# Kernel optimization log

Measured on AMD Instinct MI355X. Metric: run time of the kernel, lower is better.

## Reference

```python
import jax, jax.numpy as jnp
import numpy as np

B, L, D_IN, H = 16, 2048, 1024, 512  # bidirectional: out_size = 2*H = D_IN (k=3 SRU layout)


def setup_inputs() -> dict:
    key = jax.random.key(0)
    k1, k2, k3, k4 = jax.random.split(key, 4)
    x = jax.random.normal(k1, (B, L, D_IN), dtype=jnp.float32)
    W = jax.random.normal(k2, (D_IN, 2, H, 3), dtype=jnp.float32) * 0.02
    bf = jax.random.normal(k3, (2, H), dtype=jnp.float32) * 0.02
    br = jax.random.normal(k4, (2, H), dtype=jnp.float32) * 0.02
    return {"x": x, "W": W, "bf": bf, "br": br}


def _sru_scan(xtil, f, r, xres, reverse):
    # xtil/f/r/xres: (L, B, H). Diagonal linear recurrence:
    #   c_t = f_t * c_{t-1} + (1 - f_t) * xtil_t
    #   h_t = r_t * tanh(c_t) + (1 - r_t) * xres_t
    def step(c, inp):
        xt_, f_, r_, xr_ = inp
        c = f_ * c + (1.0 - f_) * xt_
        h = r_ * jnp.tanh(c) + (1.0 - r_) * xr_
        return c, h
    c0 = jnp.zeros(xtil.shape[1:], dtype=xtil.dtype)
    c_last, h = jax.lax.scan(step, c0, (xtil, f, r, xres), reverse=reverse)
    return h, c_last


def reference(x, W, bf, br):
    xt = jnp.transpose(x, (1, 0, 2))  # (L, B, D_IN), as the wrapper does x.transpose(0,1)
    # U: (L, B, 2 dirs, H, 3 = [x_tilde, f_pre, r_pre])
    U = jnp.einsum("lbi,idhk->lbdhk", xt, W)
    f = jax.nn.sigmoid(U[..., 1] + bf[None, None, :, :])  # (L,B,2,H)
    r = jax.nn.sigmoid(U[..., 2] + br[None, None, :, :])
    xtil = U[..., 0]
    # highway/residual: raw input split per direction since n_in == 2*H (k=3)
    xres = xt.reshape(L, B, 2, H)

    h_f, c_f = _sru_scan(xtil[:, :, 0], f[:, :, 0], r[:, :, 0], xres[:, :, 0], reverse=False)
    h_b, c_b = _sru_scan(xtil[:, :, 1], f[:, :, 1], r[:, :, 1], xres[:, :, 1], reverse=True)

    h = jnp.concatenate([h_f, h_b], axis=-1)          # (L, B, 2H)
    c = jnp.concatenate([c_f, c_b], axis=-1)          # (B, 2H) final cell states
    # wrapper returns (out.transpose(0,1), c.transpose(0,1))
    return jnp.transpose(h, (1, 0, 2)), c.T
```

## Files before the change

### kernel.cpp

```cpp
#include <hip/hip_runtime.h>
#include <stdint.h>

#define B_    16
#define L_    2048
#define DIN_  1024
#define H_    512
#define NCOL_ 3072
#define M_    (B_ * L_)
#define K_    DIN_
#define NCHUNK 16
#define CHUNK  128

typedef unsigned short u16;
typedef __bf16 bf16_t;
typedef bf16_t bf16x8 __attribute__((ext_vector_type(8)));
typedef float  f32x4  __attribute__((ext_vector_type(4)));

__device__ __forceinline__ u16 f2bf(float f) {
  union { float f; uint32_t u; } v; v.f = f;
  return (u16)((v.u + 0x7fffu + ((v.u >> 16) & 1u)) >> 16);
}
__device__ __forceinline__ float bf2f(u16 b) {
  union { uint32_t u; float f; } v; v.u = ((uint32_t)b) << 16; return v.f;
}
__device__ __forceinline__ u16 f2h(float f) {
  _Float16 h = (_Float16)f; return *(u16*)&h;
}
__device__ __forceinline__ float h2f(u16 b) {
  _Float16 h = *(_Float16*)&b; return (float)h;
}

__global__ void cvt_x_kernel(const float4* __restrict__ x, ushort4* __restrict__ xb) {
  int i = blockIdx.x * blockDim.x + threadIdx.x;
  float4 v = x[i];
  ushort4 o;
  o.x = f2bf(v.x); o.y = f2bf(v.y); o.z = f2bf(v.z); o.w = f2bf(v.w);
  xb[i] = o;
}

__global__ void transpose_w_kernel(const float* __restrict__ W, u16* __restrict__ Wt) {
  __shared__ float s[32][33];
  int n0 = blockIdx.x * 32;
  int i0 = blockIdx.y * 32;
  int tx = threadIdx.x, ty = threadIdx.y;
  #pragma unroll
  for (int y = 0; y < 32; y += 8)
    s[ty + y][tx] = W[(uint64_t)(i0 + ty + y) * NCOL_ + n0 + tx];
  __syncthreads();
  #pragma unroll
  for (int y = 0; y < 32; y += 8) {
    int n = n0 + ty + y;
    int kk = n % 3, d = n / 1536, h = (n % 1536) / 3;
    int np = kk * 1024 + d * 512 + h;
    Wt[(uint64_t)np * K_ + i0 + tx] = f2bf(s[tx][ty + y]);
  }
}

__device__ __forceinline__ void gload_lds16(const void* g, void* lds) {
  __builtin_amdgcn_global_load_lds(
      (const __attribute__((address_space(1))) uint32_t*)g,
      (__attribute__((address_space(3))) uint32_t*)lds, 16, 0, 0);
}

__device__ __forceinline__ bf16x8 lds_rd(const u16* lds, int byteOff) {
  return __builtin_bit_cast(bf16x8, *(const f32x4*)((const char*)lds + byteOff));
}

__global__ __launch_bounds__(256, 2) void gemm_u_kernel(const u16* __restrict__ A,
                                                        const u16* __restrict__ Bt,
                                                        const float* __restrict__ bfp,
                                                        const float* __restrict__ brp,
                                                        u16* __restrict__ xtilP,
                                                        u16* __restrict__ fP,
                                                        u16* __restrict__ rP) {
  __shared__ __align__(16) u16 lds[40960];

  const int bid = blockIdx.x;
  const int xcd = bid & 7;
  const int li  = bid >> 3;
  const int bm  = xcd * 32 + (li & 31);
  const int bn  = li >> 5;
  const int m0 = bm * 128, n0 = bn * 128;

  const int tid  = threadIdx.x;
  const int w    = tid >> 6, lane = tid & 63;
  const int wr   = w >> 1, wc = w & 1;
  const int rr   = lane & 15, hs = lane >> 4;
  const int swzRd = (rr & 7) << 4;
  const int hsOff = hs * 16;

  const int rStage = w * 8 + (lane >> 3);
  const int sCol   = ((lane & 7) ^ (lane >> 3)) * 8;
  const int ldsChunk = w * 1024;

  f32x4 acc[4][4] = {};

  auto stageA = [&](int bufBase, int kt) {
    #pragma unroll
    for (int j = 0; j < 4; ++j)
      gload_lds16(A + (uint64_t)(m0 + j * 32 + rStage) * K_ + kt + sCol,
                  (char*)lds + bufBase + j * 4096 + ldsChunk);
  };
  auto stageB = [&](int bufBase, int kt) {
    #pragma unroll
    for (int j = 0; j < 4; ++j)
      gload_lds16(Bt + (uint64_t)(n0 + j * 32 + rStage) * K_ + kt + sCol,
                  (char*)lds + bufBase + j * 4096 + ldsChunk);
  };

  stageA(0, 0);
  stageB(32768, 0);
  stageB(32768 + 16384, 64);
  asm volatile("s_waitcnt vmcnt(4)" ::: "memory");
  __builtin_amdgcn_sched_barrier(0);
  __builtin_amdgcn_s_barrier();

  const int aRow0 = wr * 64;
  const int bRow0 = wc * 64;

  int b3 = 0;
  #pragma unroll 1
  for (int t = 0; t < 16; ++t) {
    const int curA = (t & 1) << 14;
    const int curB = 32768 + b3 * 16384;
    const int b3n2 = (b3 >= 1) ? (b3 - 1) : 2;

    if (t < 15) stageA((~t & 1) << 14, (t + 1) * 64);
    if (t < 14) stageB(32768 + b3n2 * 16384, (t + 2) * 64);

    bf16x8 aF[4][2], bF[4][2];
    #pragma unroll
    for (int ni = 0; ni < 4; ++ni)
      #pragma unroll
      for (int ks = 0; ks < 2; ++ks)
        bF[ni][ks] = lds_rd(lds, curB + (bRow0 + ni * 16 + rr) * 128 + ((ks * 64 + hsOff) ^ swzRd));
    #pragma unroll
    for (int a = 0; a < 4; ++a)
      #pragma unroll
      for (int ks = 0; ks < 2; ++ks)
        aF[a][ks] = lds_rd(lds, curA + (aRow0 + a * 16 + rr) * 128 + ((ks * 64 + hsOff) ^ swzRd));

    #pragma unroll
    for (int a = 0; a < 4; ++a)
      #pragma unroll
      for (int ni = 0; ni < 4; ++ni)
        #pragma unroll
        for (int ks = 0; ks < 2; ++ks)
          acc[a][ni] = __builtin_amdgcn_mfma_f32_16x16x32_bf16(aF[a][ks], bF[ni][ks], acc[a][ni], 0, 0, 0);

    if (t < 14) {
      asm volatile("s_waitcnt vmcnt(4)" ::: "memory");
      __builtin_amdgcn_sched_barrier(0);
    } else if (t == 14) {
      asm volatile("s_waitcnt vmcnt(0)" ::: "memory");
      __builtin_amdgcn_sched_barrier(0);
    }
    if (t < 15) __builtin_amdgcn_s_barrier();

    b3 = (b3 + 1 == 3) ? 0 : b3 + 1;
  }

  const int kkPlane = n0 >> 10;
  const int chBase  = n0 & 1023;
  u16* plane = (kkPlane == 0) ? xtilP : (kkPlane == 1 ? fP : rP);
  const float* biasp = (kkPlane == 1) ? bfp : brp;
  #pragma unroll
  for (int mi = 0; mi < 4; ++mi) {
    #pragma unroll
    for (int ni = 0; ni < 4; ++ni) {
      const int ch = chBase + wc * 64 + ni * 16 + rr;
      const float bias = kkPlane ? biasp[ch] : 0.f;
      #pragma unroll
      for (int i = 0; i < 4; ++i) {
        const int row = m0 + wr * 64 + mi * 16 + hs * 4 + i;
        float v = acc[mi][ni][i];
        if (kkPlane) v = 1.f / (1.f + __expf(-(v + bias)));
        plane[(uint64_t)row * 1024 + ch] = f2h(v);
      }
    }
  }
}

__global__ __launch_bounds__(256) void scan_partial_kernel(const u16* __restrict__ xtilP,
                                                           const u16* __restrict__ fP,
                                                           float* __restrict__ cpart,
                                                           float* __restrict__ Pp) {
  int tid = blockIdx.x * 256 + threadIdx.x;
  int ch = tid & 1023, chunk = (tid >> 10) & (NCHUNK - 1), b = tid >> 14;
  int d = ch >> 9;
  int l = chunk * CHUNK + (d ? CHUNK - 1 : 0);
  int64_t stride = d ? -1024 : 1024;
  uint64_t base = ((uint64_t)b * L_ + l) * 1024 + ch;
  float c = 0.f, P = 1.f;
  #pragma unroll 4
  for (int it = 0; it < CHUNK; ++it) {
    float f  = h2f(fP[base]);
    float xt = h2f(xtilP[base]);
    c = f * c + (1.f - f) * xt;
    P *= f;
    base += stride;
  }
  int o = (b * NCHUNK + chunk) * 1024 + ch;
  cpart[o] = c;
  Pp[o] = P;
}

__global__ void scan_combine_kernel(const float* __restrict__ cpart, const float* __restrict__ Pp,
                                    float* __restrict__ cin, float* __restrict__ outc) {
  int tid = blockIdx.x * blockDim.x + threadIdx.x;
  int ch = tid & 1023, b = tid >> 10, d = ch >> 9;
  float c = 0.f;
  for (int i = 0; i < NCHUNK; ++i) {
    int chunk = d ? (NCHUNK - 1 - i) : i;
    int o = (b * NCHUNK + chunk) * 1024 + ch;
    cin[o] = c;
    c = cpart[o] + Pp[o] * c;
  }
  outc[ch * B_ + b] = c;
}

__global__ __launch_bounds__(256) void scan_final_kernel(const u16* __restrict__ xb,
                                                         const u16* __restrict__ xtilP,
                                                         const u16* __restrict__ fP,
                                                         const u16* __restrict__ rP,
                                                         const float* __restrict__ cin,
                                                         float* __restrict__ outh) {
  int tid = blockIdx.x * 256 + threadIdx.x;
  int ch = tid & 1023, chunk = (tid >> 10) & (NCHUNK - 1), b = tid >> 14;
  int d = ch >> 9;
  int l = chunk * CHUNK + (d ? CHUNK - 1 : 0);
  int64_t stride = d ? -1024 : 1024;
  uint64_t base = ((uint64_t)b * L_ + l) * 1024 + ch;
  float c = cin[(b * NCHUNK + chunk) * 1024 + ch];
  #pragma unroll 2
  for (int it = 0; it < CHUNK; ++it) {
    float f    = h2f(fP[base]);
    float xt   = h2f(xtilP[base]);
    float rr   = h2f(rP[base]);
    float xres = bf2f(xb[base]);
    c = f * c + (1.f - f) * xt;
    float th = 1.f - 2.f / (__expf(2.f * c) + 1.f);
    outh[base] = rr * th + (1.f - rr) * xres;
    base += stride;
  }
}

extern "C" void kernel_launch(void* const* d_in, const int* in_sizes, int n_in,
                              void* d_out, int out_size, void* d_ws, size_t ws_size,
                              hipStream_t stream) {
  const float* x   = (const float*)d_in[0];
  const float* W   = (const float*)d_in[1];
  const float* bfp = (const float*)d_in[2];
  const float* brp = (const float*)d_in[3];

  float* outh = (float*)d_out;
  float* outc = outh + (size_t)B_ * L_ * DIN_;

  u16* xb = (u16*)d_ws;
  u16* Wt = xb + (size_t)M_ * K_;
  u16* xtilP = Wt + (size_t)NCOL_ * K_;
  u16* fP    = xtilP + (size_t)M_ * 1024;
  u16* rP    = fP    + (size_t)M_ * 1024;
  float* cpart = (float*)Wt;
  float* Pp    = cpart + (size_t)B_ * NCHUNK * 1024;
  float* cin   = Pp    + (size_t)B_ * NCHUNK * 1024;

  cvt_x_kernel<<<(M_ * K_ / 4) / 256, 256, 0, stream>>>((const float4*)x, (ushort4*)xb);
  transpose_w_kernel<<<dim3(NCOL_ / 32, K_ / 32), dim3(32, 8), 0, stream>>>(W, Wt);
  gemm_u_kernel<<<(M_ / 128) * (NCOL_ / 128), 256, 0, stream>>>(xb, Wt, bfp, brp, xtilP, fP, rP);
  scan_partial_kernel<<<(B_ * NCHUNK * 1024) / 256, 256, 0, stream>>>(xtilP, fP, cpart, Pp);
  scan_combine_kernel<<<(B_ * 2 * H_) / 256, 256, 0, stream>>>(cpart, Pp, cin, outc);
  scan_final_kernel<<<(B_ * NCHUNK * 1024) / 256, 256, 0, stream>>>(xb, xtilP, fP, rP, cin, outh);
}
```

Baseline: 429.5 us.

## Enlarge GEMM block tile to 256x192 with 12 waves per block

The GEMM block tile grows from 128x128 with 4 waves to 256x192 with 12 waves (4x3 wave grid), and LDS buffers are resized to match. Staging is redistributed across the 12 waves. The epilogue now picks the output plane and bias per column, because a 192-wide tile can cross the 1024-column plane boundary. The aim is more operand reuse per global byte and fewer blocks; the cost is more LDS per block (about 136KB), which likely allows only one block per CU despite the launch_bounds(768,3) hint.

```diff
diff --git a/kernel.cpp b/kernel.cpp
--- a/kernel.cpp
+++ b/kernel.cpp
@@ -66,90 +66,89 @@
   return __builtin_bit_cast(bf16x8, *(const f32x4*)((const char*)lds + byteOff));
 }
 
-__global__ __launch_bounds__(256, 2) void gemm_u_kernel(const u16* __restrict__ A,
+__global__ __launch_bounds__(768, 3) void gemm_u_kernel(const u16* __restrict__ A,
                                                         const u16* __restrict__ Bt,
                                                         const float* __restrict__ bfp,
                                                         const float* __restrict__ brp,
                                                         u16* __restrict__ xtilP,
                                                         u16* __restrict__ fP,
                                                         u16* __restrict__ rP) {
-  __shared__ __align__(16) u16 lds[40960];
+  __shared__ __align__(16) u16 lds[69632];
 
   const int bid = blockIdx.x;
   const int xcd = bid & 7;
   const int li  = bid >> 3;
-  const int bm  = xcd * 32 + (li & 31);
-  const int bn  = li >> 5;
-  const int m0 = bm * 128, n0 = bn * 128;
+  const int bm  = xcd * 16 + (li & 15);
+  const int bn  = li >> 4;
+  const int m0 = bm * 256, n0 = bn * 192;
 
   const int tid  = threadIdx.x;
   const int w    = tid >> 6, lane = tid & 63;
-  const int wr   = w >> 1, wc = w & 1;
+  const int wr   = w >> 2;
+  const int wrM  = w & 3, wcN = w >> 2;
   const int rr   = lane & 15, hs = lane >> 4;
   const int swzRd = (rr & 7) << 4;
   const int hsOff = hs * 16;
 
-  const int rStage = w * 8 + (lane >> 3);
-  const int sCol   = ((lane & 7) ^ (lane >> 3)) * 8;
-  const int ldsChunk = w * 1024;
+  const int rSub = lane >> 3;
+  const int sCol = ((lane & 7) ^ (lane >> 3)) * 8;
 
   f32x4 acc[4][4] = {};
 
   auto stageA = [&](int bufBase, int kt) {
     #pragma unroll
-    for (int j = 0; j < 4; ++j)
-      gload_lds16(A + (uint64_t)(m0 + j * 32 + rStage) * K_ + kt + sCol,
-                  (char*)lds + bufBase + j * 4096 + ldsChunk);
+    for (int c = w; c < 32; c += 12)
+      gload_lds16(A + (uint64_t)(m0 + c * 8 + rSub) * K_ + kt + sCol,
+                  (char*)lds + bufBase + c * 1024);
   };
   auto stageB = [&](int bufBase, int kt) {
     #pragma unroll
-    for (int j = 0; j < 4; ++j)
-      gload_lds16(Bt + (uint64_t)(n0 + j * 32 + rStage) * K_ + kt + sCol,
-                  (char*)lds + bufBase + j * 4096 + ldsChunk);
+    for (int c = w; c < 24; c += 12)
+      gload_lds16(Bt + (uint64_t)(n0 + c * 8 + rSub) * K_ + kt + sCol,
+                  (char*)lds + bufBase + c * 1024);
   };
 
   stageA(0, 0);
-  stageB(32768, 0);
-  stageB(32768 + 16384, 64);
-  asm volatile("s_waitcnt vmcnt(4)" ::: "memory");
+  stageB(65536, 0);
+  stageB(65536 + 24576, 64);
+  asm volatile("s_waitcnt vmcnt(2)" ::: "memory");
   __builtin_amdgcn_sched_barrier(0);
   __builtin_amdgcn_s_barrier();
 
-  const int aRow0 = wr * 64;
-  const int bRow0 = wc * 64;
+  const int aRow0 = wrM * 64;
+  const int bRow0 = wcN * 64;
 
   int b3 = 0;
   #pragma unroll 1
   for (int t = 0; t < 16; ++t) {
-    const int curA = (t & 1) << 14;
-    const int curB = 32768 + b3 * 16384;
+    const int curA = (t & 1) << 15;
+    const int curB = 65536 + b3 * 24576;
     const int b3n2 = (b3 >= 1) ? (b3 - 1) : 2;
 
-    if (t < 15) stageA((~t & 1) << 14, (t + 1) * 64);
-    if (t < 14) stageB(32768 + b3n2 * 16384, (t + 2) * 64);
-
-    bf16x8 aF[4][2], bF[4][2];
+    if (t < 15) stageA((~t & 1) << 15, (t + 1) * 64);
+    if (t < 14) stageB(65536 + b3n2 * 24576, (t + 2) * 64);
+
+    bf16x8 bF[4][2];
     #pragma unroll
     for (int ni = 0; ni < 4; ++ni)
       #pragma unroll
       for (int ks = 0; ks < 2; ++ks)
         bF[ni][ks] = lds_rd(lds, curB + (bRow0 + ni * 16 + rr) * 128 + ((ks * 64 + hsOff) ^ swzRd));
     #pragma unroll
-    for (int a = 0; a < 4; ++a)
+    for (int a = 0; a < 4; ++a) {
+      bf16x8 aF[2];
       #pragma unroll
       for (int ks = 0; ks < 2; ++ks)
-        aF[a][ks] = lds_rd(lds, curA + (aRow0 + a * 16 + rr) * 128 + ((ks * 64 + hsOff) ^ swzRd));
-
-    #pragma unroll
-    for (int a = 0; a < 4; ++a)
+        aF[ks] = lds_rd(lds, curA + (aRow0 + a * 16 + rr) * 128 + ((ks * 64 + hsOff) ^ swzRd));
       #pragma unroll
       for (int ni = 0; ni < 4; ++ni)
         #pragma unroll
         for (int ks = 0; ks < 2; ++ks)
-          acc[a][ni] = __builtin_amdgcn_mfma_f32_16x16x32_bf16(aF[a][ks], bF[ni][ks], acc[a][ni], 0, 0, 0);
+          acc[a][ni] = __builtin_amdgcn_mfma_f32_16x16x32_bf16(aF[ks], bF[ni][ks], acc[a][ni], 0, 0, 0);
+    }
 
     if (t < 14) {
-      asm volatile("s_waitcnt vmcnt(4)" ::: "memory");
+      asm volatile("s_waitcnt vmcnt(2)" ::: "memory");
       __builtin_amdgcn_sched_barrier(0);
     } else if (t == 14) {
       asm volatile("s_waitcnt vmcnt(0)" ::: "memory");
@@ -160,21 +159,20 @@
     b3 = (b3 + 1 == 3) ? 0 : b3 + 1;
   }
 
-  const int kkPlane = n0 >> 10;
-  const int chBase  = n0 & 1023;
-  u16* plane = (kkPlane == 0) ? xtilP : (kkPlane == 1 ? fP : rP);
-  const float* biasp = (kkPlane == 1) ? bfp : brp;
   #pragma unroll
-  for (int mi = 0; mi < 4; ++mi) {
-    #pragma unroll
-    for (int ni = 0; ni < 4; ++ni) {
-      const int ch = chBase + wc * 64 + ni * 16 + rr;
-      const float bias = kkPlane ? biasp[ch] : 0.f;
+  for (int ni = 0; ni < 4; ++ni) {
+    const int col = n0 + wcN * 64 + ni * 16 + rr;
+    const int kk  = col >> 10;
+    const int ch  = col & 1023;
+    u16* plane = (kk == 0) ? xtilP : (kk == 1 ? fP : rP);
+    const float bias = kk ? ((kk == 1 ? bfp : brp)[ch]) : 0.f;
+    #pragma unroll
+    for (int mi = 0; mi < 4; ++mi) {
       #pragma unroll
       for (int i = 0; i < 4; ++i) {
-        const int row = m0 + wr * 64 + mi * 16 + hs * 4 + i;
+        const int row = m0 + wrM * 64 + mi * 16 + hs * 4 + i;
         float v = acc[mi][ni][i];
-        if (kkPlane) v = 1.f / (1.f + __expf(-(v + bias)));
+        if (kk) v = 1.f / (1.f + __expf(-(v + bias)));
         plane[(uint64_t)row * 1024 + ch] = f2h(v);
       }
     }
@@ -267,7 +265,7 @@
 
   cvt_x_kernel<<<(M_ * K_ / 4) / 256, 256, 0, stream>>>((const float4*)x, (ushort4*)xb);
   transpose_w_kernel<<<dim3(NCOL_ / 32, K_ / 32), dim3(32, 8), 0, stream>>>(W, Wt);
-  gemm_u_kernel<<<(M_ / 128) * (NCOL_ / 128), 256, 0, stream>>>(xb, Wt, bfp, brp, xtilP, fP, rP);
+  gemm_u_kernel<<<(M_ / 256) * (NCOL_ / 192), 768, 0, stream>>>(xb, Wt, bfp, brp, xtilP, fP, rP);
   scan_partial_kernel<<<(B_ * NCHUNK * 1024) / 256, 256, 0, stream>>>(xtilP, fP, cpart, Pp);
   scan_combine_kernel<<<(B_ * 2 * H_) / 256, 256, 0, stream>>>(cpart, Pp, cin, outc);
   scan_final_kernel<<<(B_ * NCHUNK * 1024) / 256, 256, 0, stream>>>(xb, xtilP, fP, rP, cin, outh);
```

Result: faster. 406.2 us (-5.4%).
